# Performance work log

Measured on AMD Instinct MI355X. Metric: run time of the kernel, lower is better.

Reference implementation:

```python
import jax, jax.numpy as jnp
import numpy as np
import math

N = 4096
E = 512          # hidden_dim
H = 8            # num_heads
MAX_STEPS = 100
D_TIME = E // 2  # 256
D_STAT = E // 4  # 128


def _time_encoding():
    # sinusoidal table [MAX_STEPS, D_TIME], matching the torch buffer
    pos = jnp.arange(MAX_STEPS, dtype=jnp.float32)[:, None]
    div = jnp.exp(jnp.arange(0, D_TIME, 2, dtype=jnp.float32) * (-math.log(10000.0) / D_TIME))
    ang = pos * div  # [MAX_STEPS, D_TIME//2]
    return jnp.stack([jnp.sin(ang), jnp.cos(ang)], axis=-1).reshape(MAX_STEPS, D_TIME)


def setup_inputs() -> dict:
    key = jax.random.key(0)
    ks = jax.random.split(key, 12)
    w = 0.02
    return {
        "x": jax.random.normal(ks[0], (N, E), jnp.float32),
        "derived_mask": jax.random.randint(ks[1], (N,), 0, 2, jnp.int32),
        "step_numbers": jax.random.randint(ks[2], (N,), 0, MAX_STEPS, jnp.int32),
        "status_embed": jax.random.normal(ks[3], (2, D_STAT), jnp.float32),
        "in_proj_w": jax.random.normal(ks[4], (3 * E, E), jnp.float32) * w,
        "in_proj_b": jnp.zeros((3 * E,), jnp.float32),
        "out_proj_w": jax.random.normal(ks[5], (E, E), jnp.float32) * w,
        "out_proj_b": jnp.zeros((E,), jnp.float32),
        "mlp_w": jax.random.normal(ks[6], (E, E + D_STAT + D_TIME), jnp.float32) * w,
        "mlp_b": jnp.zeros((E,), jnp.float32),
        "ln_gamma": jnp.ones((E,), jnp.float32),
        "ln_beta": jnp.zeros((E,), jnp.float32),
    }


def reference(x, derived_mask, step_numbers, status_embed, in_proj_w, in_proj_b,
              out_proj_w, out_proj_b, mlp_w, mlp_b, ln_gamma, ln_beta):
    n = x.shape[0]
    hd = E // H

    # --- multihead self-attention with dynamic step-based mask ---
    qkv = x @ in_proj_w.T + in_proj_b                      # [N, 3E]
    q, k, v = jnp.split(qkv, 3, axis=-1)
    q = q.reshape(n, H, hd).transpose(1, 0, 2)             # [H, N, hd]
    k = k.reshape(n, H, hd).transpose(1, 0, 2)
    v = v.reshape(n, H, hd).transpose(1, 0, 2)

    scores = jnp.einsum('hnd,hmd->hnm', q, k) / math.sqrt(hd)   # [H, N, N]
    # mask[i, j] = True  <=>  step[j] - step[i] < 0 (blocked, -inf)
    blocked = (step_numbers[None, :] - step_numbers[:, None]) < 0
    scores = jnp.where(blocked[None, :, :], jnp.float32(-1e9), scores)
    attn = jax.nn.softmax(scores, axis=-1)
    ctx = jnp.einsum('hnm,hmd->hnd', attn, v)              # [H, N, hd]
    ctx = ctx.transpose(1, 0, 2).reshape(n, E)
    x_att = ctx @ out_proj_w.T + out_proj_b                # [N, E]

    # --- embeddings ---
    status = status_embed[derived_mask]                    # [N, E/4]
    step_c = jnp.clip(step_numbers, 0, MAX_STEPS - 1)
    time_emb = _time_encoding()[step_c]                    # [N, E/2]

    # --- fused output MLP: Linear -> LayerNorm -> ReLU ---
    combined = jnp.concatenate([x_att, status, time_emb], axis=-1)  # [N, 7E/4]
    h = combined @ mlp_w.T + mlp_b                         # [N, E]
    mu = jnp.mean(h, axis=-1, keepdims=True)
    var = jnp.mean((h - mu) ** 2, axis=-1, keepdims=True)
    h = (h - mu) / jnp.sqrt(var + 1e-5) * ln_gamma + ln_beta
    out = jnp.maximum(h, 0.0)
    return x + out
```

## Files before the change

kernel.cpp:

```cpp
#include <hip/hip_runtime.h>
#include <hip/hip_bf16.h>
#include <math.h>

typedef __bf16 bf16x8 __attribute__((ext_vector_type(8)));
typedef __bf16 bf16x4 __attribute__((ext_vector_type(4)));
typedef float f32x4 __attribute__((ext_vector_type(4)));

#define N_TOK 4096
#define EDIM 512
#define NHEAD 8
#define HD 64
#define LDCOMB 896
#define NBIN 100
#define SPLITK 8
#define BK 64

#define NU_CVT 3264
#define NU_TC 64
#define NU_ADD 128
#define NU_TMAT 128
#define NB_PREP (NU_CVT + NU_TC + NU_ADD + NU_TMAT + 1)

__global__ __launch_bounds__(256) void prep_kernel(
    const float* __restrict__ x, const float* __restrict__ w_in,
    const float* __restrict__ w_mlp, const float* __restrict__ w_out,
    const float* __restrict__ status, const float* __restrict__ out_b,
    const float* __restrict__ mlp_b, const int* __restrict__ steps,
    __bf16* __restrict__ x_bf, __bf16* __restrict__ wqkv_bf,
    __bf16* __restrict__ wmlp_bf, __bf16* __restrict__ woutT_bf,
    float* __restrict__ add2, __bf16* __restrict__ tmat,
    int* __restrict__ perm, int* __restrict__ sstep,
    int* __restrict__ bs_row, int* __restrict__ qinfo) {
    __shared__ float T[64][65];
    __shared__ int hist[NBIN];
    __shared__ int offs[NBIN];
    const int bid = blockIdx.x;
    const int tid = threadIdx.x;
    const int wave = tid >> 6, lane = tid & 63;

    if (bid < NU_CVT) {
        int i = bid * 256 + tid;
        const int n0 = N_TOK * EDIM / 4;
        const int n1 = 3 * EDIM * EDIM / 4;
        const float* src; __bf16* dst;
        if (i < n0)           { src = x; dst = x_bf; }
        else if (i < n0 + n1) { i -= n0; src = w_in; dst = wqkv_bf; }
        else                  { i -= n0 + n1; src = w_mlp; dst = wmlp_bf; }
        const float4 v = ((const float4*)src)[i];
        bf16x4 o;
        o[0] = (__bf16)v.x; o[1] = (__bf16)v.y; o[2] = (__bf16)v.z; o[3] = (__bf16)v.w;
        ((bf16x4*)dst)[i] = o;
    } else if (bid < NU_CVT + NU_TC) {
        const int b2 = bid - NU_CVT;
        const int m0 = (b2 >> 3) * 64, k0 = (b2 & 7) * 64;
        const int row = tid >> 2, c4 = (tid & 3) * 16;
        #pragma unroll
        for (int i = 0; i < 4; i++) {
            const float4 v = *(const float4*)&w_out[(size_t)(m0 + row) * EDIM + k0 + c4 + i * 4];
            T[row][c4 + i * 4 + 0] = v.x;
            T[row][c4 + i * 4 + 1] = v.y;
            T[row][c4 + i * 4 + 2] = v.z;
            T[row][c4 + i * 4 + 3] = v.w;
        }
        __syncthreads();
        const int kr = tid >> 2, m16 = (tid & 3) * 16;
        bf16x8 o0, o1;
        #pragma unroll
        for (int i = 0; i < 8; i++) o0[i] = (__bf16)T[m16 + i][kr];
        #pragma unroll
        for (int i = 0; i < 8; i++) o1[i] = (__bf16)T[m16 + 8 + i][kr];
        *(bf16x8*)&woutT_bf[(size_t)(k0 + kr) * EDIM + m0 + m16] = o0;
        *(bf16x8*)&woutT_bf[(size_t)(k0 + kr) * EDIM + m0 + m16 + 8] = o1;
    } else if (bid < NU_CVT + NU_TC + NU_ADD) {
        const int j = (bid - NU_CVT - NU_TC) * 4 + wave;
        const float* wr = w_mlp + (size_t)j * LDCOMB;
        const int k8 = lane * 8;
        const float4 wa = *(const float4*)&wr[k8], wb = *(const float4*)&wr[k8 + 4];
        const float4 oa = *(const float4*)&out_b[k8], ob = *(const float4*)&out_b[k8 + 4];
        float b = wa.x * oa.x + wa.y * oa.y + wa.z * oa.z + wa.w * oa.w +
                  wb.x * ob.x + wb.y * ob.y + wb.z * ob.z + wb.w * ob.w;
        const int c2 = lane * 2;
        const float w0 = wr[EDIM + c2], w1 = wr[EDIM + c2 + 1];
        float s0 = status[c2] * w0 + status[c2 + 1] * w1;
        float s1 = status[128 + c2] * w0 + status[129 + c2] * w1;
        #pragma unroll
        for (int m = 1; m < 64; m <<= 1) {
            b += __shfl_xor(b, m);
            s0 += __shfl_xor(s0, m);
            s1 += __shfl_xor(s1, m);
        }
        if (lane == 0) {
            const float bb = b + mlp_b[j];
            add2[j] = s0 + bb;
            add2[EDIM + j] = s1 + bb;
        }
    } else if (bid < NU_CVT + NU_TC + NU_ADD + NU_TMAT) {
        const int st = bid - NU_CVT - NU_TC - NU_ADD;
        const int c = tid;
        const int pp = c >> 1;
        const float div = expf((float)(2 * pp) * (-9.210340371976184f / 256.0f));
        const float ang = (float)st * div;
        tmat[st * 256 + c] = (__bf16)((c & 1) ? cosf(ang) : sinf(ang));
    } else {
        if (tid < NBIN) hist[tid] = 0;
        __syncthreads();
        for (int i = tid; i < N_TOK; i += 256)
            atomicAdd(&hist[min(max(steps[i], 0), NBIN - 1)], 1);
        __syncthreads();
        if (tid == 0) {
            int acc = 0;
            for (int s = 0; s < NBIN; s++) { offs[s] = acc; acc += hist[s]; }
        }
        __syncthreads();
        if (tid < NBIN) hist[tid] = offs[tid];
        __syncthreads();
        for (int i = tid; i < N_TOK; i += 256) {
            const int s = min(max(steps[i], 0), NBIN - 1);
            const int pos = atomicAdd(&offs[s], 1);
            perm[pos] = i;
            sstep[pos] = s;
        }
        __syncthreads();
        for (int q = tid; q < N_TOK; q += 256)
            bs_row[q] = hist[sstep[q]];
        __syncthreads();
        for (int qt = tid; qt < 64; qt += 256) {
            qinfo[qt * 2] = bs_row[qt * 64] & ~(BK - 1);
            qinfo[qt * 2 + 1] = bs_row[qt * 64 + 63];
        }
    }
}

__global__ __launch_bounds__(256) void gemm2_kernel(const __bf16* __restrict__ x_bf,
                                                    const __bf16* __restrict__ wqkv_bf,
                                                    const float* __restrict__ b_in,
                                                    const int* __restrict__ perm,
                                                    __bf16* __restrict__ qs,
                                                    __bf16* __restrict__ ks,
                                                    __bf16* __restrict__ vt,
                                                    const __bf16* __restrict__ wmlp_bf,
                                                    const __bf16* __restrict__ woutT_bf,
                                                    __bf16* __restrict__ weff_bf,
                                                    const __bf16* __restrict__ tmat,
                                                    float* __restrict__ tv) {
    __shared__ __attribute__((aligned(16))) union {
        struct { __bf16 As[128][40]; __bf16 Bs[128][40]; } g;
        __bf16 T[128][72];
    } sm;
    __shared__ int pr[128];
    const int bid = blockIdx.x;
    const int tid = threadIdx.x;
    const int wave = tid >> 6, lane = tid & 63;
    const int wm = (wave >> 1) * 64, wn = (wave & 1) * 64;
    const int lr = lane & 15, lq = lane >> 4;

    const __bf16 *A, *B;
    int lda, ldb, bm, bn, K, mode;
    if (bid < 384) {
        A = x_bf; lda = EDIM; B = wqkv_bf; ldb = EDIM; K = EDIM; mode = 0;
        bm = (bid & 31) * 128; bn = (bid >> 5) * 128;
        if (tid < 128) pr[tid] = perm[bm + tid];
    } else if (bid < 400) {
        const int b2 = bid - 384;
        A = wmlp_bf; lda = LDCOMB; B = woutT_bf; ldb = EDIM; K = EDIM; mode = 1;
        bm = (b2 & 3) * 128; bn = (b2 >> 2) * 128;
    } else {
        const int b3 = bid - 400;
        A = tmat; lda = 256; B = wmlp_bf + 640; ldb = LDCOMB; K = 256; mode = 2;
        bm = 0; bn = b3 * 128;
    }

    f32x4 acc[4][4] = {};
    for (int k0 = 0; k0 < K; k0 += 32) {
        __syncthreads();
        #pragma unroll
        for (int c = tid; c < 512; c += 256) {
            const int row = c >> 2, k8 = (c & 3) * 8;
            const int arow = (mode == 0) ? pr[row] : (bm + row);
            *(bf16x8*)&sm.g.As[row][k8] = *(const bf16x8*)&A[(size_t)arow * lda + k0 + k8];
            *(bf16x8*)&sm.g.Bs[row][k8] = *(const bf16x8*)&B[(size_t)(bn + row) * ldb + k0 + k8];
        }
        __syncthreads();
        bf16x8 af[4], bfr[4];
        #pragma unroll
        for (int i = 0; i < 4; i++) {
            af[i]  = *(const bf16x8*)&sm.g.As[wm + i * 16 + lr][lq * 8];
            bfr[i] = *(const bf16x8*)&sm.g.Bs[wn + i * 16 + lr][lq * 8];
        }
        #pragma unroll
        for (int i = 0; i < 4; i++)
            #pragma unroll
            for (int j = 0; j < 4; j++)
                acc[i][j] = __builtin_amdgcn_mfma_f32_16x16x32_bf16(af[i], bfr[j], acc[i][j], 0, 0, 0);
    }

    if (mode == 1) {
        #pragma unroll
        for (int i = 0; i < 4; i++)
            #pragma unroll
            for (int j = 0; j < 4; j++) {
                const int col = bn + wn + j * 16 + lr;
                #pragma unroll
                for (int r = 0; r < 4; r++)
                    weff_bf[(size_t)(bm + wm + i * 16 + lq * 4 + r) * EDIM + col] =
                        (__bf16)acc[i][j][r];
            }
    } else if (mode == 2) {
        #pragma unroll
        for (int i = 0; i < 4; i++)
            #pragma unroll
            for (int j = 0; j < 4; j++) {
                const int col = bn + wn + j * 16 + lr;
                #pragma unroll
                for (int r = 0; r < 4; r++) {
                    const int row = wm + i * 16 + lq * 4 + r;
                    if (row < NBIN) tv[(size_t)row * EDIM + col] = acc[i][j][r];
                }
            }
    } else if (bn < 512) {
        const float SC = 0.125f * 1.44269504f;
        #pragma unroll
        for (int i = 0; i < 4; i++)
            #pragma unroll
            for (int j = 0; j < 4; j++) {
                const int col = bn + wn + j * 16 + lr;
                const float bv = b_in[col];
                #pragma unroll
                for (int r = 0; r < 4; r++)
                    qs[(size_t)(bm + wm + i * 16 + lq * 4 + r) * EDIM + col] =
                        (__bf16)((acc[i][j][r] + bv) * SC);
            }
    } else if (bn < 1024) {
        #pragma unroll
        for (int i = 0; i < 4; i++)
            #pragma unroll
            for (int j = 0; j < 4; j++) {
                const int col = bn + wn + j * 16 + lr;
                const float bv = b_in[col];
                #pragma unroll
                for (int r = 0; r < 4; r++)
                    ks[(size_t)(bm + wm + i * 16 + lq * 4 + r) * EDIM + (col - 512)] =
                        (__bf16)(acc[i][j][r] + bv);
            }
    } else {
        #pragma unroll
        for (int half = 0; half < 2; half++) {
            __syncthreads();
            if ((wave & 1) == half) {
                #pragma unroll
                for (int i = 0; i < 4; i++)
                    #pragma unroll
                    for (int j = 0; j < 4; j++) {
                        const float bv = b_in[bn + wn + j * 16 + lr];
                        #pragma unroll
                        for (int r = 0; r < 4; r++)
                            sm.T[wm + i * 16 + lq * 4 + r][j * 16 + lr] =
                                (__bf16)(acc[i][j][r] + bv);
                    }
            }
            __syncthreads();
            for (int u = tid; u < 1024; u += 256) {
                const int d = u & 63, t8 = (u >> 6) * 8;
                bf16x8 v;
                #pragma unroll
                for (int j = 0; j < 8; j++) v[j] = sm.T[t8 + j][d];
                const int dim = (bn - 1024) + half * 64 + d;
                *(bf16x8*)&vt[(size_t)dim * N_TOK + bm + t8] = v;
            }
        }
    }
}

__global__ __launch_bounds__(256) void attn_kernel(const __bf16* __restrict__ qs,
                                                   const __bf16* __restrict__ ks,
                                                   const __bf16* __restrict__ vt,
                                                   const int* __restrict__ bs_row,
                                                   const int* __restrict__ qinfo,
                                                   __bf16* __restrict__ po,
                                                   float* __restrict__ pl) {
    __shared__ __attribute__((aligned(16))) __bf16 Ks[BK][72];
    __shared__ __attribute__((aligned(16))) __bf16 Vs[64][BK + 8];
    __shared__ __attribute__((aligned(16))) __bf16 Ps[64][BK + 8];

    const int h = blockIdx.x & 7;
    const int qtile = (blockIdx.x >> 3) | (blockIdx.y << 3);
    const int ck = blockIdx.z;
    const int tid = threadIdx.x, wave = tid >> 6, lane = tid & 63;
    const int lr = lane & 15, lq = lane >> 4;
    const int qbase = qtile * 64 + wave * 16;

    const int kt0 = qinfo[qtile * 2];
    const int bs_blockmax = qinfo[qtile * 2 + 1];
    const int nt = (N_TOK - kt0) / BK;
    const int kta = kt0 + ((nt * ck) / SPLITK) * BK;
    const int ktb = kt0 + ((nt * (ck + 1)) / SPLITK) * BK;

    bf16x8 aq[2];
    {
        const __bf16* qrow = qs + (size_t)(qbase + lr) * EDIM + h * HD;
        aq[0] = *(const bf16x8*)&qrow[lq * 8];
        aq[1] = *(const bf16x8*)&qrow[32 + lq * 8];
    }
    int bs_r[4];
    #pragma unroll
    for (int r = 0; r < 4; r++) bs_r[r] = bs_row[qbase + lq * 4 + r];

    bf16x8 ones;
    #pragma unroll
    for (int i = 0; i < 8; i++) ones[i] = (__bf16)1.0f;

    f32x4 lacc = {};
    f32x4 o[4] = {};

    const __bf16* kbase = ks + h * HD;
    const __bf16* vbase = vt + (size_t)h * HD * N_TOK;

    const int r0 = tid >> 3, r1 = r0 + 32, k8 = (tid & 7) * 8;
    bf16x8 kr0, kr1, vr0, vr1;
    if (kta < ktb) {
        kr0 = *(const bf16x8*)&kbase[(size_t)(kta + r0) * EDIM + k8];
        kr1 = *(const bf16x8*)&kbase[(size_t)(kta + r1) * EDIM + k8];
        vr0 = *(const bf16x8*)&vbase[(size_t)r0 * N_TOK + kta + k8];
        vr1 = *(const bf16x8*)&vbase[(size_t)r1 * N_TOK + kta + k8];
    }

    for (int kt = kta; kt < ktb; kt += BK) {
        __syncthreads();
        *(bf16x8*)&Ks[r0][k8] = kr0;
        *(bf16x8*)&Ks[r1][k8] = kr1;
        *(bf16x8*)&Vs[r0][k8] = vr0;
        *(bf16x8*)&Vs[r1][k8] = vr1;
        __syncthreads();
        if (kt + BK < ktb) {
            kr0 = *(const bf16x8*)&kbase[(size_t)(kt + BK + r0) * EDIM + k8];
            kr1 = *(const bf16x8*)&kbase[(size_t)(kt + BK + r1) * EDIM + k8];
            vr0 = *(const bf16x8*)&vbase[(size_t)r0 * N_TOK + kt + BK + k8];
            vr1 = *(const bf16x8*)&vbase[(size_t)r1 * N_TOK + kt + BK + k8];
        }

        f32x4 s[4];
        #pragma unroll
        for (int t = 0; t < 4; t++) {
            bf16x8 b0 = *(const bf16x8*)&Ks[t * 16 + lr][lq * 8];
            bf16x8 b1 = *(const bf16x8*)&Ks[t * 16 + lr][32 + lq * 8];
            f32x4 a = {};
            a = __builtin_amdgcn_mfma_f32_16x16x32_bf16(aq[0], b0, a, 0, 0, 0);
            a = __builtin_amdgcn_mfma_f32_16x16x32_bf16(aq[1], b1, a, 0, 0, 0);
            s[t] = a;
        }
        if (kt < bs_blockmax) {
            #pragma unroll
            for (int t = 0; t < 4; t++) {
                const int col = kt + t * 16 + lr;
                #pragma unroll
                for (int r = 0; r < 4; r++)
                    if (col < bs_r[r]) s[t][r] = -1e9f;
            }
        }
        #pragma unroll
        for (int t = 0; t < 4; t++) {
            #pragma unroll
            for (int r = 0; r < 4; r++) {
                const float pr = exp2f(s[t][r]);
                Ps[wave * 16 + lq * 4 + r][t * 16 + lr] = (__bf16)pr;
            }
        }
        #pragma unroll
        for (int ks2 = 0; ks2 < 2; ks2++) {
            bf16x8 ap = *(const bf16x8*)&Ps[wave * 16 + lr][ks2 * 32 + lq * 8];
            lacc = __builtin_amdgcn_mfma_f32_16x16x32_bf16(ap, ones, lacc, 0, 0, 0);
            #pragma unroll
            for (int dt = 0; dt < 4; dt++) {
                bf16x8 bv = *(const bf16x8*)&Vs[dt * 16 + lr][ks2 * 32 + lq * 8];
                o[dt] = __builtin_amdgcn_mfma_f32_16x16x32_bf16(ap, bv, o[dt], 0, 0, 0);
            }
        }
    }

    __bf16* pob = po + (((size_t)(ck * NHEAD + h) * N_TOK) + qbase) * HD;
    #pragma unroll
    for (int dt = 0; dt < 4; dt++)
        #pragma unroll
        for (int r = 0; r < 4; r++)
            pob[(lq * 4 + r) * HD + dt * 16 + lr] = (__bf16)o[dt][r];
    if (lr == 0) {
        #pragma unroll
        for (int r = 0; r < 4; r++)
            pl[(size_t)(ck * NHEAD + h) * N_TOK + qbase + lq * 4 + r] = lacc[r];
    }
}

__global__ __launch_bounds__(256) void combine_kernel(const __bf16* __restrict__ po,
                                                      const float* __restrict__ pl,
                                                      const int* __restrict__ perm,
                                                      __bf16* __restrict__ ctx) {
    const int e = blockIdx.x * 256 + threadIdx.x;
    const int q = e >> 7;
    const int col = (e & 127) * 4;
    const int h = col >> 6, d = col & 63;
    float s0 = 0.f, s1 = 0.f, s2 = 0.f, s3 = 0.f, l = 0.f;
    #pragma unroll
    for (int c = 0; c < SPLITK; c++) {
        const bf16x4 v = *(const bf16x4*)&po[(((size_t)(c * NHEAD + h) * N_TOK) + q) * HD + d];
        s0 += (float)v[0]; s1 += (float)v[1]; s2 += (float)v[2]; s3 += (float)v[3];
        l += pl[(size_t)(c * NHEAD + h) * N_TOK + q];
    }
    const float rl = 1.0f / l;
    bf16x4 o;
    o[0] = (__bf16)(s0 * rl); o[1] = (__bf16)(s1 * rl);
    o[2] = (__bf16)(s2 * rl); o[3] = (__bf16)(s3 * rl);
    *(bf16x4*)&ctx[(size_t)perm[q] * EDIM + col] = o;
}

__global__ __launch_bounds__(256) void gemm_fused(const __bf16* __restrict__ A,
                                                  const __bf16* __restrict__ B,
                                                  const int* __restrict__ dmask,
                                                  const int* __restrict__ steps,
                                                  const float* __restrict__ add2,
                                                  const float* __restrict__ tv,
                                                  float* __restrict__ C) {
    __shared__ __attribute__((aligned(16))) __bf16 As[128][40];
    __shared__ __attribute__((aligned(16))) __bf16 Bs[128][40];
    const int tid = threadIdx.x;
    const int wave = tid >> 6, lane = tid & 63;
    const int wm = (wave >> 1) * 64, wn = (wave & 1) * 64;
    const int bm = blockIdx.x * 128, bn = blockIdx.y * 128;
    const int lr = lane & 15, lq = lane >> 4;

    f32x4 acc[4][4] = {};
    for (int k0 = 0; k0 < EDIM; k0 += 32) {
        __syncthreads();
        #pragma unroll
        for (int c = tid; c < 512; c += 256) {
            const int row = c >> 2, k8 = (c & 3) * 8;
            *(bf16x8*)&As[row][k8] = *(const bf16x8*)&A[(size_t)(bm + row) * EDIM + k0 + k8];
            *(bf16x8*)&Bs[row][k8] = *(const bf16x8*)&B[(size_t)(bn + row) * EDIM + k0 + k8];
        }
        __syncthreads();
        bf16x8 af[4], bfr[4];
        #pragma unroll
        for (int i = 0; i < 4; i++) {
            af[i]  = *(const bf16x8*)&As[wm + i * 16 + lr][lq * 8];
            bfr[i] = *(const bf16x8*)&Bs[wn + i * 16 + lr][lq * 8];
        }
        #pragma unroll
        for (int i = 0; i < 4; i++)
            #pragma unroll
            for (int j = 0; j < 4; j++)
                acc[i][j] = __builtin_amdgcn_mfma_f32_16x16x32_bf16(af[i], bfr[j], acc[i][j], 0, 0, 0);
    }

    int dmr[4][4], str[4][4];
    #pragma unroll
    for (int i = 0; i < 4; i++)
        #pragma unroll
        for (int r = 0; r < 4; r++) {
            const int row = bm + wm + i * 16 + lq * 4 + r;
            dmr[i][r] = dmask[row];
            str[i][r] = min(max(steps[row], 0), NBIN - 1);
        }
    #pragma unroll
    for (int i = 0; i < 4; i++)
        #pragma unroll
        for (int j = 0; j < 4; j++) {
            const int col = bn + wn + j * 16 + lr;
            #pragma unroll
            for (int r = 0; r < 4; r++) {
                const int row = bm + wm + i * 16 + lq * 4 + r;
                C[(size_t)row * EDIM + col] = acc[i][j][r]
                    + add2[dmr[i][r] * EDIM + col] + tv[str[i][r] * EDIM + col];
            }
        }
}

__global__ __launch_bounds__(256) void ln_kernel(const float* __restrict__ h,
                                                 const float* __restrict__ x,
                                                 const float* __restrict__ gamma,
                                                 const float* __restrict__ beta,
                                                 float* __restrict__ out) {
    const int row = blockIdx.x * 4 + (threadIdx.x >> 6);
    const int lane = threadIdx.x & 63;
    const float* hr = h + (size_t)row * EDIM;
    float4 v0 = ((const float4*)hr)[lane];
    float4 v1 = ((const float4*)hr)[64 + lane];
    float sum = v0.x + v0.y + v0.z + v0.w + v1.x + v1.y + v1.z + v1.w;
    float sq = v0.x * v0.x + v0.y * v0.y + v0.z * v0.z + v0.w * v0.w +
               v1.x * v1.x + v1.y * v1.y + v1.z * v1.z + v1.w * v1.w;
    #pragma unroll
    for (int m = 1; m < 64; m <<= 1) {
        sum += __shfl_xor(sum, m);
        sq  += __shfl_xor(sq, m);
    }
    const float mean = sum * (1.0f / EDIM);
    const float var = sq * (1.0f / EDIM) - mean * mean;
    const float rstd = rsqrtf(var + 1e-5f);
    const float* xr = x + (size_t)row * EDIM;
    float* orow = out + (size_t)row * EDIM;
    #pragma unroll
    for (int half = 0; half < 2; half++) {
        const float4 v = half ? v1 : v0;
        const int cb = half * 256 + lane * 4;
        const float* vp = (const float*)&v;
        float4 res;
        float tmp[4];
        #pragma unroll
        for (int i = 0; i < 4; i++) {
            const int c = cb + i;
            float t = (vp[i] - mean) * rstd * gamma[c] + beta[c];
            t = fmaxf(t, 0.f);
            tmp[i] = xr[c] + t;
        }
        res.x = tmp[0]; res.y = tmp[1]; res.z = tmp[2]; res.w = tmp[3];
        ((float4*)orow)[cb >> 2] = res;
    }
}

extern "C" void kernel_launch(void* const* d_in, const int* in_sizes, int n_in,
                              void* d_out, int out_size, void* d_ws, size_t ws_size,
                              hipStream_t stream) {
    const float* x      = (const float*)d_in[0];
    const int*   dmask  = (const int*)d_in[1];
    const int*   steps  = (const int*)d_in[2];
    const float* status = (const float*)d_in[3];
    const float* w_in   = (const float*)d_in[4];
    const float* b_in   = (const float*)d_in[5];
    const float* w_out  = (const float*)d_in[6];
    const float* b_out  = (const float*)d_in[7];
    const float* w_mlp  = (const float*)d_in[8];
    const float* b_mlp  = (const float*)d_in[9];
    const float* gamma  = (const float*)d_in[10];
    const float* beta   = (const float*)d_in[11];
    float* out = (float*)d_out;

    char* ws = (char*)d_ws;
    size_t off = 0;
    auto alloc = [&](size_t bytes) {
        void* ptr = ws + off;
        off = (off + bytes + 255) & ~(size_t)255;
        return ptr;
    };
    __bf16* x_bf    = (__bf16*)alloc((size_t)N_TOK * EDIM * 2);
    __bf16* wqkv_bf = (__bf16*)alloc((size_t)3 * EDIM * EDIM * 2);
    __bf16* wmlp_bf = (__bf16*)alloc((size_t)EDIM * LDCOMB * 2);
    __bf16* woutT_bf= (__bf16*)alloc((size_t)EDIM * EDIM * 2);
    __bf16* weff_bf = (__bf16*)alloc((size_t)EDIM * EDIM * 2);
    __bf16* qs_bf   = (__bf16*)alloc((size_t)N_TOK * EDIM * 2);
    __bf16* ks_bf   = (__bf16*)alloc((size_t)N_TOK * EDIM * 2);
    __bf16* vt_bf   = (__bf16*)alloc((size_t)EDIM * N_TOK * 2);
    __bf16* ctx_bf  = (__bf16*)alloc((size_t)N_TOK * EDIM * 2);
    float*  h_f32   = (float*)alloc((size_t)N_TOK * EDIM * 4);
    int*    perm    = (int*)alloc(N_TOK * 4);
    int*    sstep   = (int*)alloc(N_TOK * 4);
    int*    bs_row  = (int*)alloc(N_TOK * 4);
    int*    qinfo   = (int*)alloc(128 * 4);
    __bf16* po      = (__bf16*)alloc((size_t)SPLITK * NHEAD * N_TOK * HD * 2);
    float*  pl      = (float*)alloc((size_t)SPLITK * NHEAD * N_TOK * 4);
    float*  add2    = (float*)alloc(2 * EDIM * 4);
    float*  tv      = (float*)alloc((size_t)NBIN * EDIM * 4);
    __bf16* tmat    = (__bf16*)alloc(128 * 256 * 2);

    prep_kernel<<<NB_PREP, 256, 0, stream>>>(
        x, w_in, w_mlp, w_out, status, b_out, b_mlp, steps,
        x_bf, wqkv_bf, wmlp_bf, woutT_bf, add2, tmat, perm, sstep, bs_row, qinfo);
    gemm2_kernel<<<404, 256, 0, stream>>>(
        x_bf, wqkv_bf, b_in, perm, qs_bf, ks_bf, vt_bf,
        wmlp_bf, woutT_bf, weff_bf, tmat, tv);
    attn_kernel<<<dim3(64, NHEAD, SPLITK), 256, 0, stream>>>(
        qs_bf, ks_bf, vt_bf, bs_row, qinfo, po, pl);
    combine_kernel<<<(N_TOK * EDIM) / 1024, 256, 0, stream>>>(po, pl, perm, ctx_bf);
    gemm_fused<<<dim3(N_TOK / 128, EDIM / 128), 256, 0, stream>>>(
        ctx_bf, weff_bf, dmask, steps, add2, tv, h_f32);
    ln_kernel<<<N_TOK / 4, 256, 0, stream>>>(h_f32, x, gamma, beta, out);
}
```

Baseline: 192.8 us.

## Restructure attention kernel with 128-row query tiles, async LDS loads, register-resident P

The attention kernel now processes 128 query rows per block (32 per wave, two MFMA groups), so each staged K/V tile is reused by twice as many queries and the grid shrinks accordingly. K/V tiles are double-buffered and loaded directly into LDS with global_load_lds using an XOR-swizzled layout, replacing the register-staged copy and removing one barrier per iteration. Scores are computed transposed (K as the A operand), and the exp'd probabilities are packed to bf16 and rearranged across lanes with permlane32_swap and shuffles instead of round-tripping through a shared P buffer. The tradeoffs are higher register pressure, a coarser mask block range per tile (more masked work near the diagonal), and fewer blocks available to balance the load.

```diff
diff --git a/kernel.cpp b/kernel.cpp
--- a/kernel.cpp
+++ b/kernel.cpp
@@ -14,12 +14,19 @@
 #define NBIN 100
 #define SPLITK 8
 #define BK 64
+#define NQT 32
 
 #define NU_CVT 3264
 #define NU_TC 64
 #define NU_ADD 128
 #define NU_TMAT 128
 #define NB_PREP (NU_CVT + NU_TC + NU_ADD + NU_TMAT + 1)
+
+__device__ __forceinline__ unsigned int pk2(float a, float b) {
+    union { __bf16 h[2]; unsigned int u; } x;
+    x.h[0] = (__bf16)a; x.h[1] = (__bf16)b;
+    return x.u;
+}
 
 __global__ __launch_bounds__(256) void prep_kernel(
     const float* __restrict__ x, const float* __restrict__ w_in,
@@ -124,9 +131,9 @@
         for (int q = tid; q < N_TOK; q += 256)
             bs_row[q] = hist[sstep[q]];
         __syncthreads();
-        for (int qt = tid; qt < 64; qt += 256) {
-            qinfo[qt * 2] = bs_row[qt * 64] & ~(BK - 1);
-            qinfo[qt * 2 + 1] = bs_row[qt * 64 + 63];
+        for (int qt = tid; qt < NQT; qt += 256) {
+            qinfo[qt * 2] = bs_row[qt * 128] & ~(BK - 1);
+            qinfo[qt * 2 + 1] = bs_row[qt * 128 + 127];
         }
     }
 }
@@ -271,23 +278,21 @@
     }
 }
 
-__global__ __launch_bounds__(256) void attn_kernel(const __bf16* __restrict__ qs,
-                                                   const __bf16* __restrict__ ks,
-                                                   const __bf16* __restrict__ vt,
-                                                   const int* __restrict__ bs_row,
-                                                   const int* __restrict__ qinfo,
-                                                   __bf16* __restrict__ po,
-                                                   float* __restrict__ pl) {
-    __shared__ __attribute__((aligned(16))) __bf16 Ks[BK][72];
-    __shared__ __attribute__((aligned(16))) __bf16 Vs[64][BK + 8];
-    __shared__ __attribute__((aligned(16))) __bf16 Ps[64][BK + 8];
+__global__ __launch_bounds__(256, 4) void attn_kernel(const __bf16* __restrict__ qs,
+                                                      const __bf16* __restrict__ ks,
+                                                      const __bf16* __restrict__ vt,
+                                                      const int* __restrict__ bs_row,
+                                                      const int* __restrict__ qinfo,
+                                                      __bf16* __restrict__ po,
+                                                      float* __restrict__ pl) {
+    __shared__ __attribute__((aligned(16))) __bf16 KV[2][2][64 * 64];
 
     const int h = blockIdx.x & 7;
-    const int qtile = (blockIdx.x >> 3) | (blockIdx.y << 3);
-    const int ck = blockIdx.z;
+    const int qtile = blockIdx.x >> 3;
+    const int ck = blockIdx.y;
     const int tid = threadIdx.x, wave = tid >> 6, lane = tid & 63;
     const int lr = lane & 15, lq = lane >> 4;
-    const int qbase = qtile * 64 + wave * 16;
+    const int wq0 = qtile * 128 + wave * 32;
 
     const int kt0 = qinfo[qtile * 2];
     const int bs_blockmax = qinfo[qtile * 2 + 1];
@@ -295,98 +300,121 @@
     const int kta = kt0 + ((nt * ck) / SPLITK) * BK;
     const int ktb = kt0 + ((nt * (ck + 1)) / SPLITK) * BK;
 
-    bf16x8 aq[2];
-    {
-        const __bf16* qrow = qs + (size_t)(qbase + lr) * EDIM + h * HD;
-        aq[0] = *(const bf16x8*)&qrow[lq * 8];
-        aq[1] = *(const bf16x8*)&qrow[32 + lq * 8];
-    }
-    int bs_r[4];
-    #pragma unroll
-    for (int r = 0; r < 4; r++) bs_r[r] = bs_row[qbase + lq * 4 + r];
+    bf16x8 aq[2][2];
+    int bsg[2];
+    #pragma unroll
+    for (int g = 0; g < 2; g++) {
+        const __bf16* qrow = qs + (size_t)(wq0 + g * 16 + lr) * EDIM + h * HD;
+        aq[g][0] = *(const bf16x8*)&qrow[lq * 8];
+        aq[g][1] = *(const bf16x8*)&qrow[32 + lq * 8];
+        bsg[g] = bs_row[wq0 + g * 16 + lr];
+    }
 
     bf16x8 ones;
     #pragma unroll
     for (int i = 0; i < 8; i++) ones[i] = (__bf16)1.0f;
 
-    f32x4 lacc = {};
-    f32x4 o[4] = {};
-
-    const __bf16* kbase = ks + h * HD;
-    const __bf16* vbase = vt + (size_t)h * HD * N_TOK;
-
-    const int r0 = tid >> 3, r1 = r0 + 32, k8 = (tid & 7) * 8;
-    bf16x8 kr0, kr1, vr0, vr1;
-    if (kta < ktb) {
-        kr0 = *(const bf16x8*)&kbase[(size_t)(kta + r0) * EDIM + k8];
-        kr1 = *(const bf16x8*)&kbase[(size_t)(kta + r1) * EDIM + k8];
-        vr0 = *(const bf16x8*)&vbase[(size_t)r0 * N_TOK + kta + k8];
-        vr1 = *(const bf16x8*)&vbase[(size_t)r1 * N_TOK + kta + k8];
-    }
-
+    f32x4 lacc[2] = {};
+    f32x4 o[2][4] = {};
+
+    const int ro = lane >> 3;
+    const int sc = (lane & 7) ^ ro;
+    const int rbase = wave * 16;
+
+    auto stage = [&](int buf, int kt_s) {
+        #pragma unroll
+        for (int i = 0; i < 2; i++) {
+            const int rs = rbase + i * 8;
+            const __bf16* gk = ks + (size_t)(kt_s + rs + ro) * EDIM + h * HD + sc * 8;
+            __builtin_amdgcn_global_load_lds(
+                (const __attribute__((address_space(1))) unsigned int*)gk,
+                (__attribute__((address_space(3))) unsigned int*)&KV[buf][0][rs * 64],
+                16, 0, 0);
+            const __bf16* gv = vt + (size_t)(h * HD + rs + ro) * N_TOK + kt_s + sc * 8;
+            __builtin_amdgcn_global_load_lds(
+                (const __attribute__((address_space(1))) unsigned int*)gv,
+                (__attribute__((address_space(3))) unsigned int*)&KV[buf][1][rs * 64],
+                16, 0, 0);
+        }
+    };
+
+    const int cswz = lr & 7;
+    const int c0 = lq ^ cswz;
+
+    if (kta < ktb) stage(0, kta);
+    __syncthreads();
+
+    int cur = 0;
     for (int kt = kta; kt < ktb; kt += BK) {
-        __syncthreads();
-        *(bf16x8*)&Ks[r0][k8] = kr0;
-        *(bf16x8*)&Ks[r1][k8] = kr1;
-        *(bf16x8*)&Vs[r0][k8] = vr0;
-        *(bf16x8*)&Vs[r1][k8] = vr1;
-        __syncthreads();
-        if (kt + BK < ktb) {
-            kr0 = *(const bf16x8*)&kbase[(size_t)(kt + BK + r0) * EDIM + k8];
-            kr1 = *(const bf16x8*)&kbase[(size_t)(kt + BK + r1) * EDIM + k8];
-            vr0 = *(const bf16x8*)&vbase[(size_t)r0 * N_TOK + kt + BK + k8];
-            vr1 = *(const bf16x8*)&vbase[(size_t)r1 * N_TOK + kt + BK + k8];
-        }
-
-        f32x4 s[4];
+        if (kt + BK < ktb) stage(cur ^ 1, kt + BK);
+        const __bf16* Kl = &KV[cur][0][0];
+        const __bf16* Vl = &KV[cur][1][0];
+
+        unsigned int pk[2][4][2];
         #pragma unroll
         for (int t = 0; t < 4; t++) {
-            bf16x8 b0 = *(const bf16x8*)&Ks[t * 16 + lr][lq * 8];
-            bf16x8 b1 = *(const bf16x8*)&Ks[t * 16 + lr][32 + lq * 8];
-            f32x4 a = {};
-            a = __builtin_amdgcn_mfma_f32_16x16x32_bf16(aq[0], b0, a, 0, 0, 0);
-            a = __builtin_amdgcn_mfma_f32_16x16x32_bf16(aq[1], b1, a, 0, 0, 0);
-            s[t] = a;
-        }
-        if (kt < bs_blockmax) {
-            #pragma unroll
-            for (int t = 0; t < 4; t++) {
-                const int col = kt + t * 16 + lr;
-                #pragma unroll
-                for (int r = 0; r < 4; r++)
-                    if (col < bs_r[r]) s[t][r] = -1e9f;
-            }
-        }
-        #pragma unroll
-        for (int t = 0; t < 4; t++) {
-            #pragma unroll
-            for (int r = 0; r < 4; r++) {
-                const float pr = exp2f(s[t][r]);
-                Ps[wave * 16 + lq * 4 + r][t * 16 + lr] = (__bf16)pr;
-            }
-        }
-        #pragma unroll
-        for (int ks2 = 0; ks2 < 2; ks2++) {
-            bf16x8 ap = *(const bf16x8*)&Ps[wave * 16 + lr][ks2 * 32 + lq * 8];
-            lacc = __builtin_amdgcn_mfma_f32_16x16x32_bf16(ap, ones, lacc, 0, 0, 0);
+            const bf16x8 kb0 = *(const bf16x8*)&Kl[t * 1024 + lr * 64 + c0 * 8];
+            const bf16x8 kb1 = *(const bf16x8*)&Kl[t * 1024 + lr * 64 + (c0 ^ 4) * 8];
+            #pragma unroll
+            for (int g = 0; g < 2; g++) {
+                f32x4 s = {};
+                s = __builtin_amdgcn_mfma_f32_16x16x32_bf16(kb0, aq[g][0], s, 0, 0, 0);
+                s = __builtin_amdgcn_mfma_f32_16x16x32_bf16(kb1, aq[g][1], s, 0, 0, 0);
+                if (kt < bs_blockmax) {
+                    const int tokb = kt + t * 16 + lq * 4;
+                    #pragma unroll
+                    for (int r = 0; r < 4; r++)
+                        if (tokb + r < bsg[g]) s[r] = -1e9f;
+                }
+                pk[g][t][0] = pk2(exp2f(s[0]), exp2f(s[1]));
+                pk[g][t][1] = pk2(exp2f(s[2]), exp2f(s[3]));
+            }
+        }
+        #pragma unroll
+        for (int k2 = 0; k2 < 2; k2++) {
+            bf16x8 ptB[2];
+            #pragma unroll
+            for (int g = 0; g < 2; g++) {
+                unsigned int a0 = pk[g][k2 * 2][0], a1 = pk[g][k2 * 2][1];
+                unsigned int b0 = pk[g][k2 * 2 + 1][0], b1 = pk[g][k2 * 2 + 1][1];
+                asm("v_permlane32_swap_b32 %0, %1" : "+v"(a0), "+v"(b0));
+                asm("v_permlane32_swap_b32 %0, %1" : "+v"(a1), "+v"(b1));
+                const unsigned int x0 = (unsigned int)__shfl_xor((int)a0, 16);
+                const unsigned int x1 = (unsigned int)__shfl_xor((int)a1, 16);
+                const unsigned int y0 = (unsigned int)__shfl_xor((int)b0, 16);
+                const unsigned int y1 = (unsigned int)__shfl_xor((int)b1, 16);
+                union { unsigned int u[4]; bf16x8 v; } fr;
+                if (lq & 1) {
+                    fr.u[0] = y0; fr.u[1] = y1; fr.u[2] = b0; fr.u[3] = b1;
+                } else {
+                    fr.u[0] = a0; fr.u[1] = a1; fr.u[2] = x0; fr.u[3] = x1;
+                }
+                ptB[g] = fr.v;
+                lacc[g] = __builtin_amdgcn_mfma_f32_16x16x32_bf16(ones, ptB[g], lacc[g], 0, 0, 0);
+            }
             #pragma unroll
             for (int dt = 0; dt < 4; dt++) {
-                bf16x8 bv = *(const bf16x8*)&Vs[dt * 16 + lr][ks2 * 32 + lq * 8];
-                o[dt] = __builtin_amdgcn_mfma_f32_16x16x32_bf16(ap, bv, o[dt], 0, 0, 0);
-            }
-        }
-    }
-
-    __bf16* pob = po + (((size_t)(ck * NHEAD + h) * N_TOK) + qbase) * HD;
-    #pragma unroll
-    for (int dt = 0; dt < 4; dt++)
-        #pragma unroll
-        for (int r = 0; r < 4; r++)
-            pob[(lq * 4 + r) * HD + dt * 16 + lr] = (__bf16)o[dt][r];
-    if (lr == 0) {
-        #pragma unroll
-        for (int r = 0; r < 4; r++)
-            pl[(size_t)(ck * NHEAD + h) * N_TOK + qbase + lq * 4 + r] = lacc[r];
+                const bf16x8 bv = *(const bf16x8*)&Vl[dt * 1024 + lr * 64 + (c0 ^ (k2 * 4)) * 8];
+                o[0][dt] = __builtin_amdgcn_mfma_f32_16x16x32_bf16(bv, ptB[0], o[0][dt], 0, 0, 0);
+                o[1][dt] = __builtin_amdgcn_mfma_f32_16x16x32_bf16(bv, ptB[1], o[1][dt], 0, 0, 0);
+            }
+        }
+        __syncthreads();
+        cur ^= 1;
+    }
+
+    __bf16* pob = po + (((size_t)(ck * NHEAD + h) * N_TOK) + wq0) * HD;
+    #pragma unroll
+    for (int g = 0; g < 2; g++) {
+        #pragma unroll
+        for (int dt = 0; dt < 4; dt++) {
+            bf16x4 ov;
+            #pragma unroll
+            for (int r = 0; r < 4; r++) ov[r] = (__bf16)o[g][dt][r];
+            *(bf16x4*)&pob[(size_t)(g * 16 + lr) * HD + dt * 16 + lq * 4] = ov;
+        }
+        if (lq == 0)
+            pl[(size_t)(ck * NHEAD + h) * N_TOK + wq0 + g * 16 + lr] = lacc[g][0];
     }
 }
 
@@ -565,7 +593,7 @@
     gemm2_kernel<<<404, 256, 0, stream>>>(
         x_bf, wqkv_bf, b_in, perm, qs_bf, ks_bf, vt_bf,
         wmlp_bf, woutT_bf, weff_bf, tmat, tv);
-    attn_kernel<<<dim3(64, NHEAD, SPLITK), 256, 0, stream>>>(
+    attn_kernel<<<dim3(NQT * NHEAD, SPLITK), 256, 0, stream>>>(
         qs_bf, ks_bf, vt_bf, bs_row, qinfo, po, pl);
     combine_kernel<<<(N_TOK * EDIM) / 1024, 256, 0, stream>>>(po, pl, perm, ctx_bf);
     gemm_fused<<<dim3(N_TOK / 128, EDIM / 128), 256, 0, stream>>>(
```

Result: no change. 195.3 us (+1.3%).
